# Kernel tuning notes

Hardware: AMD Instinct MI355X
Metric: run time of the kernel (lower is better)

## Reference

```python
import jax, jax.numpy as jnp
import numpy as np

N_USERS = 100000
N_ITEMS = 50000
N = N_USERS + N_ITEMS
EMB_DIM = 64
N_LAYERS = 3
NNZ = 6400000
BATCH = 4096


def setup_inputs() -> dict:
    key = jax.random.key(0)
    k = jax.random.split(key, 7)
    user_emb = 0.1 * jax.random.normal(k[0], (N_USERS, EMB_DIM), dtype=jnp.float32)
    item_emb = 0.1 * jax.random.normal(k[1], (N_ITEMS, EMB_DIM), dtype=jnp.float32)
    graph_val = jax.random.uniform(k[2], (NNZ,), dtype=jnp.float32) * 0.05
    graph_src = jax.random.randint(k[3], (NNZ,), 0, N, dtype=jnp.int64) if jax.config.jax_enable_x64 else jax.random.randint(k[3], (NNZ,), 0, N).astype(jnp.int32)
    graph_dst = jax.random.randint(k[4], (NNZ,), 0, N).astype(graph_src.dtype)
    users = jax.random.randint(k[5], (BATCH,), 0, N_USERS).astype(graph_src.dtype)
    items = jax.random.randint(k[6], (BATCH,), 0, N_ITEMS).astype(graph_src.dtype)
    return {"user_emb": user_emb, "item_emb": item_emb, "graph_val": graph_val,
            "graph_src": graph_src, "graph_dst": graph_dst, "users": users, "items": items}


def _spmm(val, src, dst, x):
    # y[src] += val * x[dst]  -- sparse (COO) matrix @ dense
    return jax.ops.segment_sum(val[:, None] * x[dst], src, num_segments=N)


def reference(user_emb, item_emb, graph_val, graph_src, graph_dst, users, items):
    all_emb = jnp.concatenate([user_emb, item_emb], axis=0)  # [N, d]
    acc = all_emb  # running sum over layers (fused mean accumulation)
    x = all_emb
    for _ in range(N_LAYERS):
        x = _spmm(graph_val, graph_src, graph_dst, x)
        acc = acc + x
    light_out = acc / (N_LAYERS + 1)
    all_users = light_out[:N_USERS]
    all_items = light_out[N_USERS:]
    scores = jnp.sum(all_users[users] * all_items[items], axis=1)  # [B]
    return scores
```

## Files before the change

kernel.cpp:

```cpp
#include <hip/hip_runtime.h>


constexpr int N_USERS = 100000;
constexpr int N_ITEMS = 50000;
constexpr int N_NODES = N_USERS + N_ITEMS;
constexpr int EMB = 64;
constexpr int NNZ = 6400000;
constexpr int BATCH = 4096;

constexpr int BSHIFT = 9;
constexpr int BWIDTH = 1 << BSHIFT;
constexpr int NB = (N_NODES + BWIDTH - 1) >> BSHIFT;
constexpr int NBPAD = 512;
constexpr int BSTRIDE = 23500;
constexpr int PBSTRIDE = 36864;

constexpr int TILE = 5120;
constexpr int P1_BLOCKS = NNZ / TILE;
constexpr int EPT1 = TILE / 256;

constexpr float QSCALE = 327680.0f;
constexpr float QINV   = 1.0f / 327680.0f;

struct h4 { _Float16 x, y, z, w; };
typedef _Float16 half4v __attribute__((ext_vector_type(4)));

__global__ void gcur_init_kernel(int* __restrict__ gcur) {
    int i = blockIdx.x * blockDim.x + threadIdx.x;
    if (i < NB) gcur[i] = i * BSTRIDE;
}

__global__ void p1_bin_kernel(const int* __restrict__ src, const int* __restrict__ dst,
                              const float* __restrict__ val, int* __restrict__ gcur,
                              uint2* __restrict__ staging) {
    __shared__ int hist[NBPAD];
    __shared__ int gbase[NBPAD];
    __shared__ int cur[NBPAD];
    __shared__ int sbuf[NBPAD];
    __shared__ int lbase[NBPAD];
    __shared__ uint2 ebuf[TILE];
    int t = threadIdx.x;
    int tile = blockIdx.x * TILE;
    int srcs[EPT1];
    #pragma unroll
    for (int k = 0; k < EPT1; ++k) srcs[k] = src[tile + t + k * 256];
    for (int i = t; i < NBPAD; i += 256) { hist[i] = 0; cur[i] = 0; }
    __syncthreads();
    #pragma unroll
    for (int k = 0; k < EPT1; ++k) atomicAdd(&hist[srcs[k] >> BSHIFT], 1);
    __syncthreads();
    for (int i = t; i < NB; i += 256) {
        int h = hist[i];
        gbase[i] = (h > 0) ? atomicAdd(&gcur[i], h) : 0;
    }
    for (int i = t; i < NBPAD; i += 256) sbuf[i] = hist[i];
    __syncthreads();
    int* pin = sbuf; int* pout = lbase;
    for (int off = 1; off < NBPAD; off <<= 1) {
        for (int i = t; i < NBPAD; i += 256) {
            int v = pin[i];
            if (i >= off) v += pin[i - off];
            pout[i] = v;
        }
        __syncthreads();
        int* tmp = pin; pin = pout; pout = tmp;
    }
    for (int i = t; i < NBPAD; i += 256) lbase[i] = pin[i] - hist[i];
    __syncthreads();
    #pragma unroll
    for (int k = 0; k < EPT1; ++k) {
        int i = tile + t + k * 256;
        int s = srcs[k];
        int b = s >> BSHIFT;
        int c = atomicAdd(&cur[b], 1);
        int d = dst[i];
        float v = val[i];
        unsigned q = (unsigned)(v * QSCALE);
        if (q > 16383u) q = 16383u;
        ebuf[lbase[b] + c] = make_uint2((q << 18) | (unsigned)d, (unsigned)s);
    }
    __syncthreads();
    #pragma unroll
    for (int k = 0; k < EPT1; ++k) {
        int j = t + k * 256;
        uint2 e = ebuf[j];
        int b = (int)(e.y >> BSHIFT);
        unsigned pos = (unsigned)(gbase[b] + (j - lbase[b]));
        if (pos < (unsigned)((b + 1) * BSTRIDE))
            staging[pos] = e;
    }
}

__global__ void p2_sort_kernel(const int* __restrict__ gcur, const uint2* __restrict__ staging,
                               unsigned* __restrict__ epack, unsigned* __restrict__ prow) {
    __shared__ int hist[BWIDTH], sA[BWIDTH], sB[BWIDTH], cur[BWIDTH];
    int b = blockIdx.x;
    int t = threadIdx.x;
    int cnt = gcur[b] - b * BSTRIDE;
    if (cnt > BSTRIDE) cnt = BSTRIDE;
    int sbase = b * BSTRIDE;
    for (int i = t; i < BWIDTH; i += 256) hist[i] = 0;
    __syncthreads();
    for (int j = t; j < cnt; j += 256) {
        uint2 e = staging[sbase + j];
        atomicAdd(&hist[e.y & (BWIDTH - 1)], 1);
    }
    __syncthreads();
    for (int i = t; i < BWIDTH; i += 256) sA[i] = (hist[i] + 63) >> 6;
    __syncthreads();
    int* pin = sA; int* pout = sB;
    for (int off = 1; off < BWIDTH; off <<= 1) {
        for (int i = t; i < BWIDTH; i += 256) {
            int v = pin[i];
            if (i >= off) v += pin[i - off];
            pout[i] = v;
        }
        __syncthreads();
        int* tmp = pin; pin = pout; pout = tmp;
    }
    for (int i = t; i < BWIDTH; i += 256) {
        int pw = (hist[i] + 63) >> 6;
        int ps = pin[i] - pw;
        unsigned poff = (unsigned)(b * PBSTRIDE + 64 * ps);
        int fit = (PBSTRIDE - 64 * ps) >> 6;
        if (fit < 0) fit = 0;
        if (pw > fit) pw = fit;
        cur[i] = (int)poff;
        int node = (b << BSHIFT) + i;
        if (node < N_NODES) prow[node] = (poff << 4) | (unsigned)pw;
    }
    __syncthreads();
    unsigned bend = (unsigned)((b + 1) * PBSTRIDE);
    for (int j = t; j < cnt; j += 256) {
        uint2 e = staging[sbase + j];
        int p = atomicAdd(&cur[e.y & (BWIDTH - 1)], 1);
        if ((unsigned)p < bend) epack[p] = e.x;
    }
}

__global__ void init_kernel(const float4* __restrict__ ue, const float4* __restrict__ ie,
                            h4* __restrict__ x) {
    int i = blockIdx.x * blockDim.x + threadIdx.x;
    const int total = N_NODES * (EMB / 4);
    if (i >= total) return;
    const int usplit = N_USERS * (EMB / 4);
    float4 v = (i < usplit) ? ue[i] : ie[i - usplit];
    x[i] = h4{(_Float16)v.x, (_Float16)v.y, (_Float16)v.z, (_Float16)v.w};
}

__global__ void gather_init_kernel(const float* __restrict__ ue, const float* __restrict__ ie,
                                   const int* __restrict__ users, const int* __restrict__ items,
                                   float* __restrict__ accb) {
    int gid = blockIdx.x * blockDim.x + threadIdx.x;
    int w = gid >> 6;
    int lane = threadIdx.x & 63;
    if (w >= BATCH * 2) return;
    int b = w >> 1;
    float v;
    if (w & 1) v = ie[(long long)items[b] * EMB + lane];
    else       v = ue[(long long)users[b] * EMB + lane];
    accb[(long long)w * EMB + lane] = v;
}

__global__ void gather_add_kernel(const _Float16* __restrict__ x, const int* __restrict__ users,
                                  const int* __restrict__ items, float* __restrict__ accb) {
    int gid = blockIdx.x * blockDim.x + threadIdx.x;
    int w = gid >> 6;
    int lane = threadIdx.x & 63;
    if (w >= BATCH * 2) return;
    int b = w >> 1;
    int node = (w & 1) ? (N_USERS + items[b]) : users[b];
    accb[(long long)w * EMB + lane] += (float)x[(unsigned)node * EMB + lane];
}

__device__ __forceinline__ float dec_val(unsigned e) {
    return ((float)(e >> 18) + 0.5f) * QINV;
}

__device__ __forceinline__ void row_gather_p(unsigned pr, int lane,
                                             const unsigned* __restrict__ epack,
                                             const _Float16* __restrict__ x,
                                             float acc[4]) {
    const int sub = lane >> 4;
    const unsigned li4 = (unsigned)(lane & 15) * 4;
    float a0 = 0, a1 = 0, a2 = 0, a3 = 0;
    float b0 = 0, b1 = 0, b2 = 0, b3 = 0;
    const unsigned* ep = epack + (pr >> 4);
    int nwin = (int)(pr & 15u);
    for (int w = 0; w < nwin; ++w) {
        unsigned e = ep[lane];
        ep += 64;
        #pragma unroll
        for (int t = 0; t < 64; t += 8) {
            unsigned eA = __shfl(e, t + sub, 64);
            unsigned eB = __shfl(e, t + 4 + sub, 64);
            half4v hA = *(const half4v*)(x + ((eA & 0x3FFFFu) << 6) + li4);
            half4v hB = *(const half4v*)(x + ((eB & 0x3FFFFu) << 6) + li4);
            float vA = dec_val(eA);
            float vB = dec_val(eB);
            a0 += vA * (float)hA.x;  a1 += vA * (float)hA.y;
            a2 += vA * (float)hA.z;  a3 += vA * (float)hA.w;
            b0 += vB * (float)hB.x;  b1 += vB * (float)hB.y;
            b2 += vB * (float)hB.z;  b3 += vB * (float)hB.w;
        }
    }
    a0 += b0; a1 += b1; a2 += b2; a3 += b3;
    a0 += __shfl_xor(a0, 16, 64);  a0 += __shfl_xor(a0, 32, 64);
    a1 += __shfl_xor(a1, 16, 64);  a1 += __shfl_xor(a1, 32, 64);
    a2 += __shfl_xor(a2, 16, 64);  a2 += __shfl_xor(a2, 32, 64);
    a3 += __shfl_xor(a3, 16, 64);  a3 += __shfl_xor(a3, 32, 64);
    acc[0] = a0; acc[1] = a1; acc[2] = a2; acc[3] = a3;
}

__global__ void spmm_full_kernel(const unsigned* __restrict__ prow,
                                 const unsigned* __restrict__ epack,
                                 const _Float16* __restrict__ x, _Float16* __restrict__ y) {
    int row = blockIdx.x * (blockDim.x >> 6) + (threadIdx.x >> 6);
    int lane = threadIdx.x & 63;
    if (row >= N_NODES) return;
    float acc[4];
    row_gather_p(prow[row], lane, epack, x, acc);
    if (lane < 16) {
        half4v h = {(_Float16)acc[0], (_Float16)acc[1], (_Float16)acc[2], (_Float16)acc[3]};
        *(half4v*)(y + ((unsigned)row << 6) + (unsigned)lane * 4) = h;
    }
}

__global__ void spmm_sel_kernel(const unsigned* __restrict__ prow,
                                const unsigned* __restrict__ epack,
                                const _Float16* __restrict__ x, const int* __restrict__ users,
                                const int* __restrict__ items, float* __restrict__ accb) {
    int gid = blockIdx.x * blockDim.x + threadIdx.x;
    int w = gid >> 6;
    int lane = threadIdx.x & 63;
    if (w >= BATCH * 2) return;
    int b = w >> 1;
    int node = (w & 1) ? (N_USERS + items[b]) : users[b];
    float acc[4];
    row_gather_p(prow[node], lane, epack, x, acc);
    if (lane < 16) {
        float4* p = (float4*)(accb + ((long long)w << 6) + lane * 4);
        float4 c = *p;
        c.x += acc[0]; c.y += acc[1]; c.z += acc[2]; c.w += acc[3];
        *p = c;
    }
}

__global__ void score_kernel(const float* __restrict__ accb, float* __restrict__ out) {
    int gid = blockIdx.x * blockDim.x + threadIdx.x;
    int b = gid >> 6;
    int lane = threadIdx.x & 63;
    if (b >= BATCH) return;
    float a = accb[(long long)(2 * b) * EMB + lane];
    float c = accb[(long long)(2 * b + 1) * EMB + lane];
    float p = a * c;
    #pragma unroll
    for (int off = 32; off > 0; off >>= 1) p += __shfl_down(p, off, 64);
    if (lane == 0) out[b] = p * (1.0f / 16.0f);
}

extern "C" void kernel_launch(void* const* d_in, const int* in_sizes, int n_in,
                              void* d_out, int out_size, void* d_ws, size_t ws_size,
                              hipStream_t stream) {
    const float* user_emb  = (const float*)d_in[0];
    const float* item_emb  = (const float*)d_in[1];
    const float* graph_val = (const float*)d_in[2];
    const int*   graph_src = (const int*)d_in[3];
    const int*   graph_dst = (const int*)d_in[4];
    const int*   users     = (const int*)d_in[5];
    const int*   items     = (const int*)d_in[6];
    float* out = (float*)d_out;

    char* base = (char*)d_ws;
    const size_t STAGE_BYTES = (size_t)BSTRIDE * NB * 8;
    const size_t XBYTES = (size_t)N_NODES * EMB * 2;
    const size_t PB_SLOTS = (size_t)PBSTRIDE * NB;
    uint2*    staging = (uint2*)base;
    _Float16* A       = (_Float16*)base;
    _Float16* B       = (_Float16*)(base + XBYTES);
    float*    accb    = (float*)(base + 2 * XBYTES);
    unsigned* epack   = (unsigned*)(base + STAGE_BYTES);
    unsigned* prow    = epack + PB_SLOTS;
    int*      gcur    = (int*)(prow + N_NODES);

    const int totalv4 = N_NODES * (EMB / 4);
    const int vblocks = (totalv4 + 255) / 256;
    const int wblocks = (BATCH * 2 * 64) / 256;
    const int sblocks = (N_NODES + 3) / 4;

    hipMemsetAsync(epack, 0, PB_SLOTS * sizeof(unsigned), stream);
    gcur_init_kernel<<<(NB + 255) / 256, 256, 0, stream>>>(gcur);
    p1_bin_kernel<<<P1_BLOCKS, 256, 0, stream>>>(graph_src, graph_dst, graph_val,
                                                 gcur, staging);
    p2_sort_kernel<<<NB, 256, 0, stream>>>(gcur, staging, epack, prow);

    init_kernel<<<vblocks, 256, 0, stream>>>((const float4*)user_emb,
                                             (const float4*)item_emb, (h4*)A);
    gather_init_kernel<<<wblocks, 256, 0, stream>>>(user_emb, item_emb, users, items, accb);

    spmm_full_kernel<<<sblocks, 256, 0, stream>>>(prow, epack, A, B);
    gather_add_kernel<<<wblocks, 256, 0, stream>>>(B, users, items, accb);

    spmm_full_kernel<<<sblocks, 256, 0, stream>>>(prow, epack, B, A);
    gather_add_kernel<<<wblocks, 256, 0, stream>>>(A, users, items, accb);

    spmm_sel_kernel<<<wblocks, 256, 0, stream>>>(prow, epack, A, users, items, accb);

    score_kernel<<<(BATCH * 64) / 256, 256, 0, stream>>>(accb, out);
}
```

Baseline: 505.5 us.

## Map eight lanes per SpMM row and pad packed edge windows to eight

Each row of the sparse-dense product is now handled by an 8-lane group that loads 16-byte half8 slices, so one wavefront works on eight rows at once. Previously a full 64-lane wavefront handled one row and finished with a cross-lane reduction. Edge windows are padded to multiples of 8 instead of 64, which cuts wasted padded gathers at an average degree of about 43, and the packed bucket stride shrinks to match. The next window's edges are prefetched while the current one is processed. Risks are divergence between rows of different degree within a wavefront, and the 15-window cap, which limits a row to 120 edges.

```diff
diff --git a/kernel.cpp b/kernel.cpp
--- a/kernel.cpp
+++ b/kernel.cpp
@@ -13,7 +13,7 @@
 constexpr int NB = (N_NODES + BWIDTH - 1) >> BSHIFT;
 constexpr int NBPAD = 512;
 constexpr int BSTRIDE = 23500;
-constexpr int PBSTRIDE = 36864;
+constexpr int PBSTRIDE = 26624;
 
 constexpr int TILE = 5120;
 constexpr int P1_BLOCKS = NNZ / TILE;
@@ -23,7 +23,7 @@
 constexpr float QINV   = 1.0f / 327680.0f;
 
 struct h4 { _Float16 x, y, z, w; };
-typedef _Float16 half4v __attribute__((ext_vector_type(4)));
+typedef _Float16 half8v __attribute__((ext_vector_type(8)));
 
 __global__ void gcur_init_kernel(int* __restrict__ gcur) {
     int i = blockIdx.x * blockDim.x + threadIdx.x;
@@ -106,7 +106,7 @@
         atomicAdd(&hist[e.y & (BWIDTH - 1)], 1);
     }
     __syncthreads();
-    for (int i = t; i < BWIDTH; i += 256) sA[i] = (hist[i] + 63) >> 6;
+    for (int i = t; i < BWIDTH; i += 256) sA[i] = (hist[i] + 7) >> 3;
     __syncthreads();
     int* pin = sA; int* pout = sB;
     for (int off = 1; off < BWIDTH; off <<= 1) {
@@ -119,12 +119,13 @@
         int* tmp = pin; pin = pout; pout = tmp;
     }
     for (int i = t; i < BWIDTH; i += 256) {
-        int pw = (hist[i] + 63) >> 6;
+        int pw = (hist[i] + 7) >> 3;
         int ps = pin[i] - pw;
-        unsigned poff = (unsigned)(b * PBSTRIDE + 64 * ps);
-        int fit = (PBSTRIDE - 64 * ps) >> 6;
+        unsigned poff = (unsigned)(b * PBSTRIDE + 8 * ps);
+        int fit = (PBSTRIDE - 8 * ps) >> 3;
         if (fit < 0) fit = 0;
         if (pw > fit) pw = fit;
+        if (pw > 15) pw = 15;
         cur[i] = (int)poff;
         int node = (b << BSHIFT) + i;
         if (node < N_NODES) prow[node] = (poff << 4) | (unsigned)pw;
@@ -173,57 +174,62 @@
     accb[(long long)w * EMB + lane] += (float)x[(unsigned)node * EMB + lane];
 }
 
-__device__ __forceinline__ float dec_val(unsigned e) {
-    return ((float)(e >> 18) + 0.5f) * QINV;
-}
-
-__device__ __forceinline__ void row_gather_p(unsigned pr, int lane,
-                                             const unsigned* __restrict__ epack,
-                                             const _Float16* __restrict__ x,
-                                             float acc[4]) {
-    const int sub = lane >> 4;
-    const unsigned li4 = (unsigned)(lane & 15) * 4;
-    float a0 = 0, a1 = 0, a2 = 0, a3 = 0;
-    float b0 = 0, b1 = 0, b2 = 0, b3 = 0;
+__device__ __forceinline__ void row_gather_p8(unsigned pr, int lane,
+                                              const unsigned* __restrict__ epack,
+                                              const _Float16* __restrict__ x,
+                                              float acc[8]) {
+    const int l8 = lane & 7;
+    const int qb = lane & 56;
+    const unsigned li8b = (unsigned)l8 * 16u;
+    float a0 = 0, a1 = 0, a2 = 0, a3 = 0, a4 = 0, a5 = 0, a6 = 0, a7 = 0;
+    float b0 = 0, b1 = 0, b2 = 0, b3 = 0, b4 = 0, b5 = 0, b6 = 0, b7 = 0;
     const unsigned* ep = epack + (pr >> 4);
+    const char* xb = (const char*)x;
     int nwin = (int)(pr & 15u);
-    for (int w = 0; w < nwin; ++w) {
-        unsigned e = ep[lane];
-        ep += 64;
-        #pragma unroll
-        for (int t = 0; t < 64; t += 8) {
-            unsigned eA = __shfl(e, t + sub, 64);
-            unsigned eB = __shfl(e, t + 4 + sub, 64);
-            half4v hA = *(const half4v*)(x + ((eA & 0x3FFFFu) << 6) + li4);
-            half4v hB = *(const half4v*)(x + ((eB & 0x3FFFFu) << 6) + li4);
-            float vA = dec_val(eA);
-            float vB = dec_val(eB);
-            a0 += vA * (float)hA.x;  a1 += vA * (float)hA.y;
-            a2 += vA * (float)hA.z;  a3 += vA * (float)hA.w;
-            b0 += vB * (float)hB.x;  b1 += vB * (float)hB.y;
-            b2 += vB * (float)hB.z;  b3 += vB * (float)hB.w;
+    if (nwin > 0) {
+        unsigned e = ep[l8];
+        for (int w = 0; w < nwin; ++w) {
+            unsigned en = ep[8 + l8];
+            ep += 8;
+            unsigned voff = (e & 0x3FFFFu) << 7;
+            float v = ((float)(e >> 18) + 0.5f) * QINV;
+            #pragma unroll
+            for (int t = 0; t < 8; t += 2) {
+                unsigned offA = (unsigned)__shfl((int)voff, qb + t, 64);
+                unsigned offB = (unsigned)__shfl((int)voff, qb + t + 1, 64);
+                float vA = __shfl(v, qb + t, 64);
+                float vB = __shfl(v, qb + t + 1, 64);
+                const half8v hA = *(const half8v*)(xb + (offA | li8b));
+                const half8v hB = *(const half8v*)(xb + (offB | li8b));
+                a0 += vA * (float)hA[0];  a1 += vA * (float)hA[1];
+                a2 += vA * (float)hA[2];  a3 += vA * (float)hA[3];
+                a4 += vA * (float)hA[4];  a5 += vA * (float)hA[5];
+                a6 += vA * (float)hA[6];  a7 += vA * (float)hA[7];
+                b0 += vB * (float)hB[0];  b1 += vB * (float)hB[1];
+                b2 += vB * (float)hB[2];  b3 += vB * (float)hB[3];
+                b4 += vB * (float)hB[4];  b5 += vB * (float)hB[5];
+                b6 += vB * (float)hB[6];  b7 += vB * (float)hB[7];
+            }
+            e = en;
         }
     }
-    a0 += b0; a1 += b1; a2 += b2; a3 += b3;
-    a0 += __shfl_xor(a0, 16, 64);  a0 += __shfl_xor(a0, 32, 64);
-    a1 += __shfl_xor(a1, 16, 64);  a1 += __shfl_xor(a1, 32, 64);
-    a2 += __shfl_xor(a2, 16, 64);  a2 += __shfl_xor(a2, 32, 64);
-    a3 += __shfl_xor(a3, 16, 64);  a3 += __shfl_xor(a3, 32, 64);
-    acc[0] = a0; acc[1] = a1; acc[2] = a2; acc[3] = a3;
+    acc[0] = a0 + b0; acc[1] = a1 + b1; acc[2] = a2 + b2; acc[3] = a3 + b3;
+    acc[4] = a4 + b4; acc[5] = a5 + b5; acc[6] = a6 + b6; acc[7] = a7 + b7;
 }
 
 __global__ void spmm_full_kernel(const unsigned* __restrict__ prow,
                                  const unsigned* __restrict__ epack,
                                  const _Float16* __restrict__ x, _Float16* __restrict__ y) {
-    int row = blockIdx.x * (blockDim.x >> 6) + (threadIdx.x >> 6);
-    int lane = threadIdx.x & 63;
+    int gid = blockIdx.x * blockDim.x + threadIdx.x;
+    int row = gid >> 3;
     if (row >= N_NODES) return;
-    float acc[4];
-    row_gather_p(prow[row], lane, epack, x, acc);
-    if (lane < 16) {
-        half4v h = {(_Float16)acc[0], (_Float16)acc[1], (_Float16)acc[2], (_Float16)acc[3]};
-        *(half4v*)(y + ((unsigned)row << 6) + (unsigned)lane * 4) = h;
-    }
+    int lane = threadIdx.x & 63;
+    float acc[8];
+    row_gather_p8(prow[row], lane, epack, x, acc);
+    half8v h;
+    #pragma unroll
+    for (int i = 0; i < 8; ++i) h[i] = (_Float16)acc[i];
+    *(half8v*)(y + ((unsigned)row << 6) + (unsigned)(lane & 7) * 8) = h;
 }
 
 __global__ void spmm_sel_kernel(const unsigned* __restrict__ prow,
@@ -231,19 +237,18 @@
                                 const _Float16* __restrict__ x, const int* __restrict__ users,
                                 const int* __restrict__ items, float* __restrict__ accb) {
     int gid = blockIdx.x * blockDim.x + threadIdx.x;
-    int w = gid >> 6;
-    int lane = threadIdx.x & 63;
-    if (w >= BATCH * 2) return;
-    int b = w >> 1;
-    int node = (w & 1) ? (N_USERS + items[b]) : users[b];
-    float acc[4];
-    row_gather_p(prow[node], lane, epack, x, acc);
-    if (lane < 16) {
-        float4* p = (float4*)(accb + ((long long)w << 6) + lane * 4);
-        float4 c = *p;
-        c.x += acc[0]; c.y += acc[1]; c.z += acc[2]; c.w += acc[3];
-        *p = c;
-    }
+    int g = gid >> 3;
+    if (g >= BATCH * 2) return;
+    int lane = threadIdx.x & 63;
+    int b = g >> 1;
+    int node = (g & 1) ? (N_USERS + items[b]) : users[b];
+    float acc[8];
+    row_gather_p8(prow[node], lane, epack, x, acc);
+    float4* p = (float4*)(accb + ((long long)g << 6) + (lane & 7) * 8);
+    float4 c0 = p[0], c1 = p[1];
+    c0.x += acc[0]; c0.y += acc[1]; c0.z += acc[2]; c0.w += acc[3];
+    c1.x += acc[4]; c1.y += acc[5]; c1.z += acc[6]; c1.w += acc[7];
+    p[0] = c0; p[1] = c1;
 }
 
 __global__ void score_kernel(const float* __restrict__ accb, float* __restrict__ out) {
@@ -286,7 +291,8 @@
     const int totalv4 = N_NODES * (EMB / 4);
     const int vblocks = (totalv4 + 255) / 256;
     const int wblocks = (BATCH * 2 * 64) / 256;
-    const int sblocks = (N_NODES + 3) / 4;
+    const int sblocks = (N_NODES * 8 + 255) / 256;
+    const int selblocks = (BATCH * 2 * 8) / 256;
 
     hipMemsetAsync(epack, 0, PB_SLOTS * sizeof(unsigned), stream);
     gcur_init_kernel<<<(NB + 255) / 256, 256, 0, stream>>>(gcur);
@@ -304,7 +310,7 @@
     spmm_full_kernel<<<sblocks, 256, 0, stream>>>(prow, epack, B, A);
     gather_add_kernel<<<wblocks, 256, 0, stream>>>(A, users, items, accb);
 
-    spmm_sel_kernel<<<wblocks, 256, 0, stream>>>(prow, epack, A, users, items, accb);
+    spmm_sel_kernel<<<selblocks, 256, 0, stream>>>(prow, epack, A, users, items, accb);
 
     score_kernel<<<(BATCH * 64) / 256, 256, 0, stream>>>(accb, out);
 }
```

Measured after the change: 521.3 us. 3.1% more time.
